# Kernel tuning notes

Hardware: AMD Instinct MI355X
Metric: run time of the kernel (lower is better)

## Reference

```python
import jax, jax.numpy as jnp
import numpy as np

N = 100000
E = 1600000
B = 64
NUM_CLASSES = 10


def setup_inputs() -> dict:
    key = jax.random.key(0)
    ks = jax.random.split(key, 8)
    x = jax.random.normal(ks[0], (N, 5), dtype=jnp.float32)
    edge_index = jax.random.randint(ks[1], (2, E), 0, N, dtype=jnp.int64)
    batch = jnp.sort(jax.random.randint(ks[2], (N,), 0, B, dtype=jnp.int64))

    def glorot(k, fan_in, fan_out):
        s = jnp.sqrt(6.0 / (fan_in + fan_out)).astype(jnp.float32)
        return jax.random.uniform(k, (fan_in, fan_out), jnp.float32, -s, s)

    dims = [(5, 32), (32, 64), (64, 128), (128, 256)]
    Ws = [glorot(jax.random.fold_in(ks[3], i), a, b) for i, (a, b) in enumerate(dims)]
    bs = [jnp.zeros((b,), jnp.float32) for (_, b) in dims]
    fc1_w = glorot(ks[4], 256, 100)
    fc1_b = jnp.zeros((100,), jnp.float32)
    fc2_w = glorot(ks[5], 100, NUM_CLASSES)
    fc2_b = jnp.zeros((NUM_CLASSES,), jnp.float32)
    return {
        'x': x, 'edge_index': edge_index, 'batch': batch,
        'W1': Ws[0], 'b1': bs[0], 'W2': Ws[1], 'b2': bs[1],
        'W3': Ws[2], 'b3': bs[2], 'W4': Ws[3], 'b4': bs[3],
        'fc1_w': fc1_w, 'fc1_b': fc1_b, 'fc2_w': fc2_w, 'fc2_b': fc2_b,
    }


def _gcn_conv(x, W, b, src, dst, dinv):
    h = x @ W                                   # [N, out]
    norm = (dinv[src] * dinv[dst])[:, None]      # [E, 1]
    msg = h[src] * norm                          # gather + scale
    agg = jax.ops.segment_sum(msg, dst, num_segments=N)
    agg = agg + h * (dinv * dinv)[:, None]       # self-loop contribution
    return agg + b


def reference(x, edge_index, batch, W1, b1, W2, b2, W3, b3, W4, b4,
              fc1_w, fc1_b, fc2_w, fc2_b):
    src, dst = edge_index[0], edge_index[1]
    # degree including self-loop
    deg = jax.ops.segment_sum(jnp.ones((E,), jnp.float32), dst, num_segments=N) + 1.0
    dinv = jax.lax.rsqrt(deg)

    h = jax.nn.relu(_gcn_conv(x, W1, b1, src, dst, dinv))
    # mesh_unpool with pool target 0 -> identity
    h = jax.nn.relu(_gcn_conv(h, W2, b2, src, dst, dinv))
    h = jax.nn.relu(_gcn_conv(h, W3, b3, src, dst, dinv))
    h = jax.nn.relu(_gcn_conv(h, W4, b4, src, dst, dinv))

    # global mean pool over graphs
    sums = jax.ops.segment_sum(h, batch, num_segments=B)
    cnt = jax.ops.segment_sum(jnp.ones((N,), jnp.float32), batch, num_segments=B)
    pooled = sums / jnp.maximum(cnt, 1.0)[:, None]

    h = jax.nn.relu(pooled @ fc1_w + fc1_b)
    return jax.nn.log_softmax(h @ fc2_w + fc2_b, axis=-1)
```

## Files before the change

kernel.cpp:

```cpp
#include <hip/hip_runtime.h>
#include <hip/hip_bf16.h>
#include <cmath>

#define NN 100000
#define NE 1600000
#define NBATCH 64
#define NB 391
#define NBP 512
#define BCAP 5120
#define NPAD (NB * BCAP)

typedef __attribute__((ext_vector_type(8))) _Float16 f16x8;
typedef __attribute__((ext_vector_type(4))) float f32x4;
typedef __attribute__((ext_vector_type(2))) float f32x2;

__device__ __forceinline__ void atomAdd(float* p, float v) {
  unsafeAtomicAdd(p, v);
}

__device__ __forceinline__ unsigned char f2fp8(float f) {
  int pk = __builtin_amdgcn_cvt_pk_fp8_f32(f, f, 0, false);
  return (unsigned char)(pk & 0xff);
}

__device__ __forceinline__ void fp8x16_to_f16(uint4 v, _Float16* h) {
  f32x2 t;
  t = __builtin_amdgcn_cvt_pk_f32_fp8(v.x, false); h[0] = (_Float16)t.x;  h[1] = (_Float16)t.y;
  t = __builtin_amdgcn_cvt_pk_f32_fp8(v.x, true);  h[2] = (_Float16)t.x;  h[3] = (_Float16)t.y;
  t = __builtin_amdgcn_cvt_pk_f32_fp8(v.y, false); h[4] = (_Float16)t.x;  h[5] = (_Float16)t.y;
  t = __builtin_amdgcn_cvt_pk_f32_fp8(v.y, true);  h[6] = (_Float16)t.x;  h[7] = (_Float16)t.y;
  t = __builtin_amdgcn_cvt_pk_f32_fp8(v.z, false); h[8] = (_Float16)t.x;  h[9] = (_Float16)t.y;
  t = __builtin_amdgcn_cvt_pk_f32_fp8(v.z, true);  h[10] = (_Float16)t.x; h[11] = (_Float16)t.y;
  t = __builtin_amdgcn_cvt_pk_f32_fp8(v.w, false); h[12] = (_Float16)t.x; h[13] = (_Float16)t.y;
  t = __builtin_amdgcn_cvt_pk_f32_fp8(v.w, true);  h[14] = (_Float16)t.x; h[15] = (_Float16)t.y;
}

__global__ __launch_bounds__(256) void k_bin(const int* __restrict__ src,
    const int* __restrict__ dst, int* __restrict__ bucketCnt, unsigned* __restrict__ pairs,
    const float* __restrict__ W2, const float* __restrict__ W3, const float* __restrict__ W4,
    _Float16* __restrict__ Wt2, _Float16* __restrict__ Wt3, _Float16* __restrict__ Wt4) {
  __shared__ int hist[NBP];
  __shared__ int scn[NBP];
  __shared__ int ofs[NBP];
  __shared__ int gbase[NBP];
  __shared__ unsigned buf[4096];
  __shared__ unsigned short bufb[4096];
  const int base = blockIdx.x * 4096;
  const int n = (NE - base < 4096) ? NE - base : 4096;
  for (int i = threadIdx.x; i < NBP; i += 256) hist[i] = 0;
  __syncthreads();

  int myS[16], myD[16];
  int nloc = 0;
  for (int i = threadIdx.x, j = 0; i < n; i += 256, ++j) {
    myS[j] = src[base + i];
    myD[j] = dst[base + i];
    atomicAdd(&hist[myD[j] >> 8], 1);
    nloc = j + 1;
  }
  __syncthreads();

  scn[threadIdx.x] = hist[threadIdx.x];
  scn[threadIdx.x + 256] = hist[threadIdx.x + 256];
  __syncthreads();
  for (int off = 1; off < NBP; off <<= 1) {
    const int i0 = threadIdx.x, i1 = threadIdx.x + 256;
    int t0 = (i0 >= off) ? scn[i0 - off] : 0;
    int t1 = (i1 >= off) ? scn[i1 - off] : 0;
    __syncthreads();
    scn[i0] += t0;
    scn[i1] += t1;
    __syncthreads();
  }
  ofs[threadIdx.x] = scn[threadIdx.x] - hist[threadIdx.x];
  ofs[threadIdx.x + 256] = scn[threadIdx.x + 256] - hist[threadIdx.x + 256];
  for (int b = threadIdx.x; b < NB; b += 256) {
    int c = hist[b];
    if (c) gbase[b] = b * BCAP + atomicAdd(&bucketCnt[b], c);
  }
  __syncthreads();

  for (int j = 0; j < nloc; ++j) {
    int b = myD[j] >> 8;
    int slot = atomicAdd(&ofs[b], 1);
    buf[slot] = ((unsigned)myS[j] << 8) | ((unsigned)myD[j] & 255u);
    bufb[slot] = (unsigned short)b;
  }
  __syncthreads();

  for (int i = threadIdx.x; i < n; i += 256) {
    int b = (int)bufb[i];
    int ex = scn[b] - hist[b];
    pairs[gbase[b] + (i - ex)] = buf[i];
  }

  int idx = blockIdx.x * 256 + threadIdx.x;
  if (idx < 2048) {
    int k = idx / 64, m = idx - k * 64;
    Wt2[m * 32 + k] = (_Float16)W2[idx];
  } else if (idx < 10240) {
    int j = idx - 2048;
    int k = j / 128, m = j - k * 128;
    Wt3[m * 64 + k] = (_Float16)W3[j];
  } else if (idx < 43008) {
    int j = idx - 10240;
    int k = j / 256, m = j - k * 256;
    Wt4[m * 128 + k] = (_Float16)W4[j];
  }
}

__global__ __launch_bounds__(256) void k_cntfill(const unsigned* __restrict__ pairs,
    const int* __restrict__ bucketCnt, const int* __restrict__ batch,
    const float* __restrict__ x, int* __restrict__ rowbeg, int* __restrict__ rowend,
    float* __restrict__ dinv, int* __restrict__ csrc, float* __restrict__ pcnt,
    _Float16* __restrict__ xs8) {
  __shared__ int c[256];
  __shared__ int scn[256];
  __shared__ int rowb[256];
  __shared__ int ofs[256];
  __shared__ int h[64];
  const int tid = threadIdx.x;
  c[tid] = 0; ofs[tid] = 0;
  if (tid < 64) h[tid] = 0;
  __syncthreads();
  const int b = blockIdx.x;
  const int s = b * BCAP;
  const int e = s + bucketCnt[b];
  for (int i = s + tid; i < e; i += 256) atomicAdd(&c[pairs[i] & 255u], 1);
  __syncthreads();
  const int v = c[tid];
  scn[tid] = v;
  __syncthreads();
  for (int off = 1; off < 256; off <<= 1) {
    int t = (tid >= off) ? scn[tid - off] : 0;
    __syncthreads();
    scn[tid] += t;
    __syncthreads();
  }
  rowb[tid] = s + scn[tid] - v;
  const int node = b * 256 + tid;
  rowbeg[node] = rowb[tid];
  rowend[node] = rowb[tid] + v;
  if (node < NN) {
    const float di = rsqrtf((float)v + 1.0f);
    dinv[node] = di;
    f16x8 o = {0, 0, 0, 0, 0, 0, 0, 0};
    o[0] = (_Float16)(x[(size_t)node * 5 + 0] * di);
    o[1] = (_Float16)(x[(size_t)node * 5 + 1] * di);
    o[2] = (_Float16)(x[(size_t)node * 5 + 2] * di);
    o[3] = (_Float16)(x[(size_t)node * 5 + 3] * di);
    o[4] = (_Float16)(x[(size_t)node * 5 + 4] * di);
    *(f16x8*)(xs8 + (size_t)node * 8) = o;
    atomicAdd(&h[batch[node]], 1);
  }
  __syncthreads();
  for (int i = s + tid; i < e; i += 256) {
    unsigned p = pairs[i];
    int t = (int)(p & 255u);
    int pos = rowb[t] + atomicAdd(&ofs[t], 1);
    csrc[pos] = (int)(p >> 8);
  }
  if (tid < 64 && h[tid]) atomAdd(&pcnt[tid], (float)h[tid]);
}

struct MegaArgs {
  const _Float16* xs8;
  const int* rowbeg; const int* rowend; const int* csrc;
  const float* dinv;
  const float* W1; const float* b1;
  unsigned char* F0;
  const _Float16* Wt2; const float* b2;
  unsigned char* F1;
  const _Float16* Wt3; const float* b3;
  unsigned char* F2;
  const _Float16* Wt4; const float* b4;
  unsigned char* AG8;
  const int* batch; float* pooled; const float* pcnt;
  const float* fc1w; const float* fc1b; const float* fc2w; const float* fc2b;
  float* out;
};

__global__ __launch_bounds__(256) void kw_l1(MegaArgs a) {
  __shared__ float w_s[160];
  __shared__ float b_s[32];
  const int tid = threadIdx.x;
  if (tid < 160) w_s[tid] = a.W1[tid];
  if (tid < 32) b_s[tid] = a.b1[tid];
  __syncthreads();
  const int r = blockIdx.x * 256 + tid;
  if (r >= NN) return;
  const float di = a.dinv[r];
  f16x8 av = *(const f16x8*)(a.xs8 + (size_t)r * 8);
  f16x8 cacc = {0, 0, 0, 0, 0, 0, 0, 0};
  int e = a.rowbeg[r];
  const int e1 = a.rowend[r];
  for (; e + 2 <= e1; e += 2) {
    const int s0 = a.csrc[e], s1 = a.csrc[e + 1];
    av   += *(const f16x8*)(a.xs8 + (size_t)s0 * 8);
    cacc += *(const f16x8*)(a.xs8 + (size_t)s1 * 8);
  }
  if (e < e1) av += *(const f16x8*)(a.xs8 + (size_t)a.csrc[e] * 8);
  av += cacc;
  const float f0 = (float)av[0] * di, f1 = (float)av[1] * di, f2 = (float)av[2] * di,
              f3 = (float)av[3] * di, f4 = (float)av[4] * di;
  float v[32];
#pragma unroll
  for (int j = 0; j < 32; ++j) {
    float s = b_s[j] + f0 * w_s[j] + f1 * w_s[32 + j] + f2 * w_s[64 + j]
                     + f3 * w_s[96 + j] + f4 * w_s[128 + j];
    v[j] = fmaxf(s, 0.f) * di;
  }
  unsigned u[8];
#pragma unroll
  for (int g2 = 0; g2 < 8; ++g2) {
    int uu = 0;
    uu = __builtin_amdgcn_cvt_pk_fp8_f32(v[4 * g2],     v[4 * g2 + 1], uu, false);
    uu = __builtin_amdgcn_cvt_pk_fp8_f32(v[4 * g2 + 2], v[4 * g2 + 3], uu, true);
    u[g2] = (unsigned)uu;
  }
  uint4* op = (uint4*)(a.F0 + (size_t)r * 32);
  op[0] = make_uint4(u[0], u[1], u[2], u[3]);
  op[1] = make_uint4(u[4], u[5], u[6], u[7]);
}

template<int K>
__global__ __launch_bounds__(256) void kw_gather8(const unsigned char* __restrict__ in,
    MegaArgs a) {
  constexpr int TPR = K / 16;
  constexpr int RPB = 256 / TPR;
  const int r = blockIdx.x * RPB + threadIdx.x / TPR;
  if (r >= NN) return;
  const int c = (threadIdx.x % TPR) * 16;
  const float di = a.dinv[r];
  f32x2 acc[8];
  {
    const uint4 v = *(const uint4*)(in + (size_t)r * K + c);
    acc[0] = __builtin_amdgcn_cvt_pk_f32_fp8(v.x, false);
    acc[1] = __builtin_amdgcn_cvt_pk_f32_fp8(v.x, true);
    acc[2] = __builtin_amdgcn_cvt_pk_f32_fp8(v.y, false);
    acc[3] = __builtin_amdgcn_cvt_pk_f32_fp8(v.y, true);
    acc[4] = __builtin_amdgcn_cvt_pk_f32_fp8(v.z, false);
    acc[5] = __builtin_amdgcn_cvt_pk_f32_fp8(v.z, true);
    acc[6] = __builtin_amdgcn_cvt_pk_f32_fp8(v.w, false);
    acc[7] = __builtin_amdgcn_cvt_pk_f32_fp8(v.w, true);
  }
  int e = a.rowbeg[r];
  const int e1 = a.rowend[r];
  for (; e + 2 <= e1; e += 2) {
    const int s0 = a.csrc[e], s1 = a.csrc[e + 1];
    const uint4 v0 = *(const uint4*)(in + (size_t)s0 * K + c);
    const uint4 v1 = *(const uint4*)(in + (size_t)s1 * K + c);
    acc[0] += __builtin_amdgcn_cvt_pk_f32_fp8(v0.x, false);
    acc[1] += __builtin_amdgcn_cvt_pk_f32_fp8(v0.x, true);
    acc[2] += __builtin_amdgcn_cvt_pk_f32_fp8(v0.y, false);
    acc[3] += __builtin_amdgcn_cvt_pk_f32_fp8(v0.y, true);
    acc[4] += __builtin_amdgcn_cvt_pk_f32_fp8(v0.z, false);
    acc[5] += __builtin_amdgcn_cvt_pk_f32_fp8(v0.z, true);
    acc[6] += __builtin_amdgcn_cvt_pk_f32_fp8(v0.w, false);
    acc[7] += __builtin_amdgcn_cvt_pk_f32_fp8(v0.w, true);
    acc[0] += __builtin_amdgcn_cvt_pk_f32_fp8(v1.x, false);
    acc[1] += __builtin_amdgcn_cvt_pk_f32_fp8(v1.x, true);
    acc[2] += __builtin_amdgcn_cvt_pk_f32_fp8(v1.y, false);
    acc[3] += __builtin_amdgcn_cvt_pk_f32_fp8(v1.y, true);
    acc[4] += __builtin_amdgcn_cvt_pk_f32_fp8(v1.z, false);
    acc[5] += __builtin_amdgcn_cvt_pk_f32_fp8(v1.z, true);
    acc[6] += __builtin_amdgcn_cvt_pk_f32_fp8(v1.w, false);
    acc[7] += __builtin_amdgcn_cvt_pk_f32_fp8(v1.w, true);
  }
  if (e < e1) {
    const uint4 v0 = *(const uint4*)(in + (size_t)a.csrc[e] * K + c);
    acc[0] += __builtin_amdgcn_cvt_pk_f32_fp8(v0.x, false);
    acc[1] += __builtin_amdgcn_cvt_pk_f32_fp8(v0.x, true);
    acc[2] += __builtin_amdgcn_cvt_pk_f32_fp8(v0.y, false);
    acc[3] += __builtin_amdgcn_cvt_pk_f32_fp8(v0.y, true);
    acc[4] += __builtin_amdgcn_cvt_pk_f32_fp8(v0.z, false);
    acc[5] += __builtin_amdgcn_cvt_pk_f32_fp8(v0.z, true);
    acc[6] += __builtin_amdgcn_cvt_pk_f32_fp8(v0.w, false);
    acc[7] += __builtin_amdgcn_cvt_pk_f32_fp8(v0.w, true);
  }
  int w0 = 0, w1 = 0, w2 = 0, w3 = 0;
  w0 = __builtin_amdgcn_cvt_pk_fp8_f32(acc[0].x * di, acc[0].y * di, 0, false);
  w0 = __builtin_amdgcn_cvt_pk_fp8_f32(acc[1].x * di, acc[1].y * di, w0, true);
  w1 = __builtin_amdgcn_cvt_pk_fp8_f32(acc[2].x * di, acc[2].y * di, 0, false);
  w1 = __builtin_amdgcn_cvt_pk_fp8_f32(acc[3].x * di, acc[3].y * di, w1, true);
  w2 = __builtin_amdgcn_cvt_pk_fp8_f32(acc[4].x * di, acc[4].y * di, 0, false);
  w2 = __builtin_amdgcn_cvt_pk_fp8_f32(acc[5].x * di, acc[5].y * di, w2, true);
  w3 = __builtin_amdgcn_cvt_pk_fp8_f32(acc[6].x * di, acc[6].y * di, 0, false);
  w3 = __builtin_amdgcn_cvt_pk_fp8_f32(acc[7].x * di, acc[7].y * di, w3, true);
  *(uint4*)(a.AG8 + (size_t)r * K + c) = make_uint4((unsigned)w0, (unsigned)w1,
                                                    (unsigned)w2, (unsigned)w3);
}

template<int K, int M, int MODE>
__global__ __launch_bounds__(256) void kw_gemm(MegaArgs a,
    const _Float16* __restrict__ Wt, const float* __restrict__ bias,
    unsigned char* __restrict__ outp) {
  constexpr int KC = 32;
  constexpr int KP = K + 8;
  constexpr int WP = KC + 8;
  constexpr int CTW = M / 64;
  constexpr int C16 = K / 16;
  __shared__ _Float16 a_s[64 * KP];
  __shared__ _Float16 w_s[M * WP];
  const int tid = threadIdx.x;
  const int wave = tid >> 6, lane = tid & 63;
  const int m16 = lane & 15, q = lane >> 4;
  const int r0 = blockIdx.x * 64;

  for (int idx = tid; idx < 64 * C16; idx += 256) {
    int row = idx / C16, cc = (idx % C16) * 16;
    uint4 v = {0u, 0u, 0u, 0u};
    if (r0 + row < NN) v = *(const uint4*)(a.AG8 + (size_t)(r0 + row) * K + cc);
    _Float16 h[16];
    fp8x16_to_f16(v, h);
    *(uint4*)&a_s[row * KP + cc]     = *(uint4*)&h[0];
    *(uint4*)&a_s[row * KP + cc + 8] = *(uint4*)&h[8];
  }
  f32x4 acc[4][CTW];
#pragma unroll
  for (int rt = 0; rt < 4; ++rt)
#pragma unroll
    for (int ct = 0; ct < CTW; ++ct) acc[rt][ct] = (f32x4){0.f, 0.f, 0.f, 0.f};

  for (int kc = 0; kc < K; kc += KC) {
    __syncthreads();
    for (int idx = tid; idx < M * (KC / 8); idx += 256) {
      int m = idx / (KC / 8), cc = (idx % (KC / 8)) * 8;
      uint4 v = *(const uint4*)(Wt + (size_t)m * K + kc + cc);
      *(uint4*)&w_s[m * WP + cc] = v;
    }
    __syncthreads();
    f16x8 bfr[CTW];
#pragma unroll
    for (int ct = 0; ct < CTW; ++ct)
      bfr[ct] = *(const f16x8*)&w_s[(wave * (M / 4) + ct * 16 + m16) * WP + q * 8];
#pragma unroll
    for (int rt = 0; rt < 4; ++rt) {
      f16x8 afr = *(const f16x8*)&a_s[(rt * 16 + m16) * KP + kc + q * 8];
#pragma unroll
      for (int ct = 0; ct < CTW; ++ct)
        acc[rt][ct] = __builtin_amdgcn_mfma_f32_16x16x32_f16(afr, bfr[ct], acc[rt][ct], 0, 0, 0);
    }
  }

  if constexpr (MODE == 1) {
    const int rlast = (r0 + 63 < NN) ? r0 + 63 : NN - 1;
    const int bmin = a.batch[r0];
    const int bmax = a.batch[rlast];
    int rowb[4][4];
#pragma unroll
    for (int rt = 0; rt < 4; ++rt)
#pragma unroll
      for (int reg = 0; reg < 4; ++reg) {
        const int row = r0 + rt * 16 + q * 4 + reg;
        rowb[rt][reg] = (row < NN) ? a.batch[row] : -1;
      }
#pragma unroll
    for (int ct = 0; ct < CTW; ++ct) {
      const int col = wave * (M / 4) + ct * 16 + m16;
      const float bv = bias[col];
      for (int b = bmin; b <= bmax; ++b) {
        float s = 0.f;
#pragma unroll
        for (int rt = 0; rt < 4; ++rt)
#pragma unroll
          for (int reg = 0; reg < 4; ++reg)
            if (rowb[rt][reg] == b) s += fmaxf(acc[rt][ct][reg] + bv, 0.f);
        s += __shfl_xor(s, 16);
        s += __shfl_xor(s, 32);
        if (q == 0) atomAdd(&a.pooled[b * M + col], s);
      }
    }
  } else {
    float dsc[4][4];
#pragma unroll
    for (int rt = 0; rt < 4; ++rt)
#pragma unroll
      for (int reg = 0; reg < 4; ++reg) {
        const int row = r0 + rt * 16 + q * 4 + reg;
        dsc[rt][reg] = (row < NN) ? a.dinv[row] : 0.f;
      }
#pragma unroll
    for (int rt = 0; rt < 4; ++rt) {
#pragma unroll
      for (int ct = 0; ct < CTW; ++ct) {
        const int col = wave * (M / 4) + ct * 16 + m16;
        const float bv = bias[col];
#pragma unroll
        for (int reg = 0; reg < 4; ++reg) {
          const int row = r0 + rt * 16 + q * 4 + reg;
          if (row < NN) {
            float vv = fmaxf(acc[rt][ct][reg] + bv, 0.f) * dsc[rt][reg];
            outp[(size_t)row * M + col] = f2fp8(vv);
          }
        }
      }
    }
  }
}

__global__ __launch_bounds__(256) void kw_mlp(MegaArgs a) {
  __shared__ float p[256];
  __shared__ float h1[100];
  __shared__ float lo[10];
  const int tid = threadIdx.x;
  const int b = blockIdx.x;
  const float inv = 1.0f / fmaxf(a.pcnt[b], 1.0f);
  p[tid] = a.pooled[b * 256 + tid] * inv;
  __syncthreads();
  for (int j = tid; j < 100; j += 256) {
    float s = a.fc1b[j];
    for (int k = 0; k < 256; ++k) s += p[k] * a.fc1w[k * 100 + j];
    h1[j] = fmaxf(s, 0.f);
  }
  __syncthreads();
  if (tid < 10) {
    float s = a.fc2b[tid];
    for (int k = 0; k < 100; ++k) s += h1[k] * a.fc2w[k * 10 + tid];
    lo[tid] = s;
  }
  __syncthreads();
  if (tid == 0) {
    float m = lo[0];
    for (int j = 1; j < 10; ++j) m = fmaxf(m, lo[j]);
    float ssum = 0.f;
    for (int j = 0; j < 10; ++j) ssum += expf(lo[j] - m);
    float lse = m + logf(ssum);
    for (int j = 0; j < 10; ++j) a.out[b * 10 + j] = lo[j] - lse;
  }
}

extern "C" void kernel_launch(void* const* d_in, const int* in_sizes, int n_in,
                              void* d_out, int out_size, void* d_ws, size_t ws_size,
                              hipStream_t stream) {
  const float* x     = (const float*)d_in[0];
  const int*   ei    = (const int*)d_in[1];
  const int*   batch = (const int*)d_in[2];
  const float* W1 = (const float*)d_in[3];  const float* b1 = (const float*)d_in[4];
  const float* W2 = (const float*)d_in[5];  const float* b2 = (const float*)d_in[6];
  const float* W3 = (const float*)d_in[7];  const float* b3 = (const float*)d_in[8];
  const float* W4 = (const float*)d_in[9];  const float* b4 = (const float*)d_in[10];
  const float* fc1w = (const float*)d_in[11]; const float* fc1b = (const float*)d_in[12];
  const float* fc2w = (const float*)d_in[13]; const float* fc2b = (const float*)d_in[14];
  float* out = (float*)d_out;

  const int* src = ei;
  const int* dst = ei + NE;

  float* ws = (float*)d_ws;
  float* pooled = ws;
  float* pcnt   = pooled + 16384;
  int*   bucketCnt = (int*)(pcnt + 64);
  float* dinv   = (float*)(bucketCnt + 512);
  int*   rowbeg = (int*)(dinv + 100352);
  int*   rowend = rowbeg + 100352;
  int*   csrc   = rowend + 100352;
  unsigned* pairs = (unsigned*)(csrc + NPAD);
  _Float16* xs8 = (_Float16*)(pairs + NPAD);
  unsigned char* F0 = (unsigned char*)(xs8 + 800768);
  unsigned char* F1 = F0 + 3200000;
  unsigned char* F2 = F1 + 6400000;
  unsigned char* AG8 = F2 + 12800000;
  _Float16* Wt2 = (_Float16*)(AG8 + 12800000);
  _Float16* Wt3 = Wt2 + 32 * 64;
  _Float16* Wt4 = Wt3 + 64 * 128;

  (void)hipMemsetAsync(pooled, 0, (16384 + 64 + 512) * sizeof(float), stream);
  k_bin<<<(NE + 4095) / 4096, 256, 0, stream>>>(src, dst, bucketCnt, pairs,
                                                W2, W3, W4, Wt2, Wt3, Wt4);
  k_cntfill<<<NB, 256, 0, stream>>>(pairs, bucketCnt, batch, x,
                                    rowbeg, rowend, dinv, csrc, pcnt, xs8);

  MegaArgs m;
  m.xs8 = xs8; m.rowbeg = rowbeg; m.rowend = rowend; m.csrc = csrc;
  m.dinv = dinv;
  m.W1 = W1; m.b1 = b1; m.F0 = F0;
  m.Wt2 = Wt2; m.b2 = b2; m.F1 = F1;
  m.Wt3 = Wt3; m.b3 = b3; m.F2 = F2;
  m.Wt4 = Wt4; m.b4 = b4; m.AG8 = AG8;
  m.batch = batch; m.pooled = pooled; m.pcnt = pcnt;
  m.fc1w = fc1w; m.fc1b = fc1b; m.fc2w = fc2w; m.fc2b = fc2b;
  m.out = out;

  kw_l1<<<(NN + 255) / 256, 256, 0, stream>>>(m);
  kw_gather8<32><<<(NN + 127) / 128, 256, 0, stream>>>(F0, m);
  kw_gemm<32, 64, 0><<<(NN + 63) / 64, 256, 0, stream>>>(m, Wt2, b2, F1);
  kw_gather8<64><<<(NN + 63) / 64, 256, 0, stream>>>(F1, m);
  kw_gemm<64, 128, 0><<<(NN + 63) / 64, 256, 0, stream>>>(m, Wt3, b3, F2);
  kw_gather8<128><<<(NN + 31) / 32, 256, 0, stream>>>(F2, m);
  kw_gemm<128, 256, 1><<<(NN + 63) / 64, 256, 0, stream>>>(m, Wt4, b4, nullptr);
  kw_mlp<<<NBATCH, 256, 0, stream>>>(m);
}
```

Before: 280.2 us.

## Fuse neighbor aggregation gather into GEMM A-tile load, drop AG8 buffer

The separate gather kernels that summed fp8 neighbor features and wrote an fp8 aggregate buffer are merged into the GEMM kernel. Each GEMM block now gathers and accumulates its 64 rows directly, with 4 threads per row, and writes f16 straight into shared memory. This removes three kernel launches, the aggregate buffer's write and re-read, and one fp8 requantization step. The cost is fewer threads per row for the irregular gather (4 per row, each loading up to 32 bytes), and gather latency now shares occupancy with the GEMM's shared memory.

```diff
diff --git a/kernel.cpp b/kernel.cpp
--- a/kernel.cpp
+++ b/kernel.cpp
@@ -23,16 +23,26 @@
   return (unsigned char)(pk & 0xff);
 }
 
-__device__ __forceinline__ void fp8x16_to_f16(uint4 v, _Float16* h) {
-  f32x2 t;
-  t = __builtin_amdgcn_cvt_pk_f32_fp8(v.x, false); h[0] = (_Float16)t.x;  h[1] = (_Float16)t.y;
-  t = __builtin_amdgcn_cvt_pk_f32_fp8(v.x, true);  h[2] = (_Float16)t.x;  h[3] = (_Float16)t.y;
-  t = __builtin_amdgcn_cvt_pk_f32_fp8(v.y, false); h[4] = (_Float16)t.x;  h[5] = (_Float16)t.y;
-  t = __builtin_amdgcn_cvt_pk_f32_fp8(v.y, true);  h[6] = (_Float16)t.x;  h[7] = (_Float16)t.y;
-  t = __builtin_amdgcn_cvt_pk_f32_fp8(v.z, false); h[8] = (_Float16)t.x;  h[9] = (_Float16)t.y;
-  t = __builtin_amdgcn_cvt_pk_f32_fp8(v.z, true);  h[10] = (_Float16)t.x; h[11] = (_Float16)t.y;
-  t = __builtin_amdgcn_cvt_pk_f32_fp8(v.w, false); h[12] = (_Float16)t.x; h[13] = (_Float16)t.y;
-  t = __builtin_amdgcn_cvt_pk_f32_fp8(v.w, true);  h[14] = (_Float16)t.x; h[15] = (_Float16)t.y;
+template<int W32>
+__device__ __forceinline__ void ldw(const unsigned char* p, unsigned* v) {
+  if constexpr (W32 == 2) {
+    uint2 t = *(const uint2*)p; v[0] = t.x; v[1] = t.y;
+  } else if constexpr (W32 == 4) {
+    uint4 t = *(const uint4*)p; v[0] = t.x; v[1] = t.y; v[2] = t.z; v[3] = t.w;
+  } else {
+    uint4 t0 = *(const uint4*)p; uint4 t1 = *(const uint4*)(p + 16);
+    v[0] = t0.x; v[1] = t0.y; v[2] = t0.z; v[3] = t0.w;
+    v[4] = t1.x; v[5] = t1.y; v[6] = t1.z; v[7] = t1.w;
+  }
+}
+
+template<int W32>
+__device__ __forceinline__ void accw(const unsigned* v, f32x2* acc) {
+#pragma unroll
+  for (int w = 0; w < W32; ++w) {
+    acc[2 * w]     += __builtin_amdgcn_cvt_pk_f32_fp8(v[w], false);
+    acc[2 * w + 1] += __builtin_amdgcn_cvt_pk_f32_fp8(v[w], true);
+  }
 }
 
 __global__ __launch_bounds__(256) void k_bin(const int* __restrict__ src,
@@ -174,7 +184,6 @@
   const _Float16* Wt3; const float* b3;
   unsigned char* F2;
   const _Float16* Wt4; const float* b4;
-  unsigned char* AG8;
   const int* batch; float* pooled; const float* pcnt;
   const float* fc1w; const float* fc1b; const float* fc2w; const float* fc2b;
   float* out;
@@ -223,83 +232,17 @@
   op[1] = make_uint4(u[4], u[5], u[6], u[7]);
 }
 
-template<int K>
-__global__ __launch_bounds__(256) void kw_gather8(const unsigned char* __restrict__ in,
-    MegaArgs a) {
-  constexpr int TPR = K / 16;
-  constexpr int RPB = 256 / TPR;
-  const int r = blockIdx.x * RPB + threadIdx.x / TPR;
-  if (r >= NN) return;
-  const int c = (threadIdx.x % TPR) * 16;
-  const float di = a.dinv[r];
-  f32x2 acc[8];
-  {
-    const uint4 v = *(const uint4*)(in + (size_t)r * K + c);
-    acc[0] = __builtin_amdgcn_cvt_pk_f32_fp8(v.x, false);
-    acc[1] = __builtin_amdgcn_cvt_pk_f32_fp8(v.x, true);
-    acc[2] = __builtin_amdgcn_cvt_pk_f32_fp8(v.y, false);
-    acc[3] = __builtin_amdgcn_cvt_pk_f32_fp8(v.y, true);
-    acc[4] = __builtin_amdgcn_cvt_pk_f32_fp8(v.z, false);
-    acc[5] = __builtin_amdgcn_cvt_pk_f32_fp8(v.z, true);
-    acc[6] = __builtin_amdgcn_cvt_pk_f32_fp8(v.w, false);
-    acc[7] = __builtin_amdgcn_cvt_pk_f32_fp8(v.w, true);
-  }
-  int e = a.rowbeg[r];
-  const int e1 = a.rowend[r];
-  for (; e + 2 <= e1; e += 2) {
-    const int s0 = a.csrc[e], s1 = a.csrc[e + 1];
-    const uint4 v0 = *(const uint4*)(in + (size_t)s0 * K + c);
-    const uint4 v1 = *(const uint4*)(in + (size_t)s1 * K + c);
-    acc[0] += __builtin_amdgcn_cvt_pk_f32_fp8(v0.x, false);
-    acc[1] += __builtin_amdgcn_cvt_pk_f32_fp8(v0.x, true);
-    acc[2] += __builtin_amdgcn_cvt_pk_f32_fp8(v0.y, false);
-    acc[3] += __builtin_amdgcn_cvt_pk_f32_fp8(v0.y, true);
-    acc[4] += __builtin_amdgcn_cvt_pk_f32_fp8(v0.z, false);
-    acc[5] += __builtin_amdgcn_cvt_pk_f32_fp8(v0.z, true);
-    acc[6] += __builtin_amdgcn_cvt_pk_f32_fp8(v0.w, false);
-    acc[7] += __builtin_amdgcn_cvt_pk_f32_fp8(v0.w, true);
-    acc[0] += __builtin_amdgcn_cvt_pk_f32_fp8(v1.x, false);
-    acc[1] += __builtin_amdgcn_cvt_pk_f32_fp8(v1.x, true);
-    acc[2] += __builtin_amdgcn_cvt_pk_f32_fp8(v1.y, false);
-    acc[3] += __builtin_amdgcn_cvt_pk_f32_fp8(v1.y, true);
-    acc[4] += __builtin_amdgcn_cvt_pk_f32_fp8(v1.z, false);
-    acc[5] += __builtin_amdgcn_cvt_pk_f32_fp8(v1.z, true);
-    acc[6] += __builtin_amdgcn_cvt_pk_f32_fp8(v1.w, false);
-    acc[7] += __builtin_amdgcn_cvt_pk_f32_fp8(v1.w, true);
-  }
-  if (e < e1) {
-    const uint4 v0 = *(const uint4*)(in + (size_t)a.csrc[e] * K + c);
-    acc[0] += __builtin_amdgcn_cvt_pk_f32_fp8(v0.x, false);
-    acc[1] += __builtin_amdgcn_cvt_pk_f32_fp8(v0.x, true);
-    acc[2] += __builtin_amdgcn_cvt_pk_f32_fp8(v0.y, false);
-    acc[3] += __builtin_amdgcn_cvt_pk_f32_fp8(v0.y, true);
-    acc[4] += __builtin_amdgcn_cvt_pk_f32_fp8(v0.z, false);
-    acc[5] += __builtin_amdgcn_cvt_pk_f32_fp8(v0.z, true);
-    acc[6] += __builtin_amdgcn_cvt_pk_f32_fp8(v0.w, false);
-    acc[7] += __builtin_amdgcn_cvt_pk_f32_fp8(v0.w, true);
-  }
-  int w0 = 0, w1 = 0, w2 = 0, w3 = 0;
-  w0 = __builtin_amdgcn_cvt_pk_fp8_f32(acc[0].x * di, acc[0].y * di, 0, false);
-  w0 = __builtin_amdgcn_cvt_pk_fp8_f32(acc[1].x * di, acc[1].y * di, w0, true);
-  w1 = __builtin_amdgcn_cvt_pk_fp8_f32(acc[2].x * di, acc[2].y * di, 0, false);
-  w1 = __builtin_amdgcn_cvt_pk_fp8_f32(acc[3].x * di, acc[3].y * di, w1, true);
-  w2 = __builtin_amdgcn_cvt_pk_fp8_f32(acc[4].x * di, acc[4].y * di, 0, false);
-  w2 = __builtin_amdgcn_cvt_pk_fp8_f32(acc[5].x * di, acc[5].y * di, w2, true);
-  w3 = __builtin_amdgcn_cvt_pk_fp8_f32(acc[6].x * di, acc[6].y * di, 0, false);
-  w3 = __builtin_amdgcn_cvt_pk_fp8_f32(acc[7].x * di, acc[7].y * di, w3, true);
-  *(uint4*)(a.AG8 + (size_t)r * K + c) = make_uint4((unsigned)w0, (unsigned)w1,
-                                                    (unsigned)w2, (unsigned)w3);
-}
-
 template<int K, int M, int MODE>
-__global__ __launch_bounds__(256) void kw_gemm(MegaArgs a,
+__global__ __launch_bounds__(256) void kw_fgemm(MegaArgs a,
+    const unsigned char* __restrict__ in,
     const _Float16* __restrict__ Wt, const float* __restrict__ bias,
     unsigned char* __restrict__ outp) {
   constexpr int KC = 32;
   constexpr int KP = K + 8;
   constexpr int WP = KC + 8;
   constexpr int CTW = M / 64;
-  constexpr int C16 = K / 16;
+  constexpr int CB = K / 4;
+  constexpr int W32 = CB / 4;
   __shared__ _Float16 a_s[64 * KP];
   __shared__ _Float16 w_s[M * WP];
   const int tid = threadIdx.x;
@@ -307,15 +250,44 @@
   const int m16 = lane & 15, q = lane >> 4;
   const int r0 = blockIdx.x * 64;
 
-  for (int idx = tid; idx < 64 * C16; idx += 256) {
-    int row = idx / C16, cc = (idx % C16) * 16;
-    uint4 v = {0u, 0u, 0u, 0u};
-    if (r0 + row < NN) v = *(const uint4*)(a.AG8 + (size_t)(r0 + row) * K + cc);
-    _Float16 h[16];
-    fp8x16_to_f16(v, h);
-    *(uint4*)&a_s[row * KP + cc]     = *(uint4*)&h[0];
-    *(uint4*)&a_s[row * KP + cc + 8] = *(uint4*)&h[8];
-  }
+  {
+    const int row = tid >> 2;
+    const int c = (tid & 3) * CB;
+    const int r = r0 + row;
+    f32x2 acc[2 * W32];
+#pragma unroll
+    for (int i = 0; i < 2 * W32; ++i) acc[i] = (f32x2){0.f, 0.f};
+    float di = 0.f;
+    if (r < NN) {
+      di = a.dinv[r];
+      unsigned v0[W32], v1[W32];
+      ldw<W32>(in + (size_t)r * K + c, v0);
+      accw<W32>(v0, acc);
+      int e = a.rowbeg[r];
+      const int e1 = a.rowend[r];
+      for (; e + 2 <= e1; e += 2) {
+        const int s0 = a.csrc[e], s1 = a.csrc[e + 1];
+        ldw<W32>(in + (size_t)s0 * K + c, v0);
+        ldw<W32>(in + (size_t)s1 * K + c, v1);
+        accw<W32>(v0, acc);
+        accw<W32>(v1, acc);
+      }
+      if (e < e1) {
+        ldw<W32>(in + (size_t)a.csrc[e] * K + c, v0);
+        accw<W32>(v0, acc);
+      }
+    }
+    _Float16 h[CB];
+#pragma unroll
+    for (int i = 0; i < 2 * W32; ++i) {
+      h[2 * i]     = (_Float16)(acc[i].x * di);
+      h[2 * i + 1] = (_Float16)(acc[i].y * di);
+    }
+#pragma unroll
+    for (int i = 0; i < CB / 8; ++i)
+      *(uint4*)&a_s[row * KP + c + i * 8] = *(uint4*)&h[i * 8];
+  }
+
   f32x4 acc[4][CTW];
 #pragma unroll
   for (int rt = 0; rt < 4; ++rt)
@@ -460,8 +432,7 @@
   unsigned char* F0 = (unsigned char*)(xs8 + 800768);
   unsigned char* F1 = F0 + 3200000;
   unsigned char* F2 = F1 + 6400000;
-  unsigned char* AG8 = F2 + 12800000;
-  _Float16* Wt2 = (_Float16*)(AG8 + 12800000);
+  _Float16* Wt2 = (_Float16*)(F2 + 12800000);
   _Float16* Wt3 = Wt2 + 32 * 64;
   _Float16* Wt4 = Wt3 + 64 * 128;
 
@@ -477,17 +448,14 @@
   m.W1 = W1; m.b1 = b1; m.F0 = F0;
   m.Wt2 = Wt2; m.b2 = b2; m.F1 = F1;
   m.Wt3 = Wt3; m.b3 = b3; m.F2 = F2;
-  m.Wt4 = Wt4; m.b4 = b4; m.AG8 = AG8;
+  m.Wt4 = Wt4; m.b4 = b4;
   m.batch = batch; m.pooled = pooled; m.pcnt = pcnt;
   m.fc1w = fc1w; m.fc1b = fc1b; m.fc2w = fc2w; m.fc2b = fc2b;
   m.out = out;
 
   kw_l1<<<(NN + 255) / 256, 256, 0, stream>>>(m);
-  kw_gather8<32><<<(NN + 127) / 128, 256, 0, stream>>>(F0, m);
-  kw_gemm<32, 64, 0><<<(NN + 63) / 64, 256, 0, stream>>>(m, Wt2, b2, F1);
-  kw_gather8<64><<<(NN + 63) / 64, 256, 0, stream>>>(F1, m);
-  kw_gemm<64, 128, 0><<<(NN + 63) / 64, 256, 0, stream>>>(m, Wt3, b3, F2);
-  kw_gather8<128><<<(NN + 31) / 32, 256, 0, stream>>>(F2, m);
-  kw_gemm<128, 256, 1><<<(NN + 63) / 64, 256, 0, stream>>>(m, Wt4, b4, nullptr);
+  kw_fgemm<32, 64, 0><<<(NN + 63) / 64, 256, 0, stream>>>(m, F0, Wt2, b2, F1);
+  kw_fgemm<64, 128, 0><<<(NN + 63) / 64, 256, 0, stream>>>(m, F1, Wt3, b3, F2);
+  kw_fgemm<128, 256, 1><<<(NN + 63) / 64, 256, 0, stream>>>(m, F2, Wt4, b4, nullptr);
   kw_mlp<<<NBATCH, 256, 0, stream>>>(m);
 }
```

New measurement: 289.2 us. 3.2% more time.
